# Kernel optimization log

Measured on AMD Instinct MI355X. Metric: run time of the kernel, lower is better.

Reference implementation:

```python
import jax, jax.numpy as jnp
import numpy as np

N_BLOCKS = 12   # grid rows == cols
D = 256         # per-block feature size (small -> memory-bound)
BATCH = 8192    # samples per block

# Deterministic block-sparse pattern: block (i, j) is active iff (i - j) % 3 == 0.
_mask = np.array([[(i - j) % 3 == 0 for j in range(N_BLOCKS)] for i in range(N_BLOCKS)])
_I, _J = np.nonzero(_mask)  # 48 active blocks
N_ACTIVE = _I.shape[0]


def setup_inputs() -> dict:
    key = jax.random.key(0)
    k1, k2, k3 = jax.random.split(key, 3)
    X = jax.random.normal(k1, (N_BLOCKS, BATCH, D), dtype=jnp.float32)
    # One Linear(D, D) per active block: weight [K, D_in, D_out], bias [K, D_out]
    W = jax.random.normal(k2, (N_ACTIVE, D, D), dtype=jnp.float32) / np.sqrt(D).astype(np.float32)
    b = jax.random.normal(k3, (N_ACTIVE, D), dtype=jnp.float32) * 0.01
    i_idx = jnp.asarray(_I, dtype=jnp.int32)  # output-row index of each active block
    j_idx = jnpim if False else jnp.asarray(_J, dtype=jnp.int32)  # input-col index of each active block
    return {"X": X, "W": W, "b": b, "i_idx": i_idx, "j_idx": j_idx}


def reference(X, W, b, i_idx, j_idx):
    # Gather the input block feeding each active sub-module: [K, BATCH, D]
    Xg = X[j_idx]
    # Apply each block's Linear in one batched contraction: [K, BATCH, D]
    h = jnp.einsum('kbi,kio->kbo', Xg, W) + b[:, None, :]
    # Sum block outputs into their output rows (the '+' combiner / safe_sum):
    # rows with no active block get an all-zero output, matching the zero-vector semantics.
    y = jax.ops.segment_sum(h, i_idx, num_segments=N_BLOCKS)  # [N_BLOCKS, BATCH, D]
    return y
```

## Files before the change

kernel.cpp:

```cpp
#include <hip/hip_runtime.h>

#define N_BLOCKS 12
#define D 256
#define BATCH 8192

typedef __attribute__((ext_vector_type(8))) short bf16x8;
typedef __attribute__((ext_vector_type(16))) float f32x16;

__device__ __forceinline__ unsigned short f2bf(float f) {
  unsigned int u = __float_as_uint(f);
  u += 0x7fffu + ((u >> 16) & 1u);
  return (unsigned short)(u >> 16);
}

__device__ __forceinline__ void gld16(const unsigned short* g, unsigned short* l) {
  __builtin_amdgcn_global_load_lds(
      (const __attribute__((address_space(1))) unsigned int*)g,
      (__attribute__((address_space(3))) unsigned int*)l,
      16, 0, 0);
}

__global__ void cvt_x(const float* __restrict__ X, unsigned short* __restrict__ Xb) {
  const long long t = (long long)blockIdx.x * 256 + threadIdx.x;
  const long long base = t * 8;
  const float4 v0 = *(const float4*)(X + base);
  const float4 v1 = *(const float4*)(X + base + 4);
  uint4 r;
  r.x = (unsigned)f2bf(v0.x) | ((unsigned)f2bf(v0.y) << 16);
  r.y = (unsigned)f2bf(v0.z) | ((unsigned)f2bf(v0.w) << 16);
  r.z = (unsigned)f2bf(v1.x) | ((unsigned)f2bf(v1.y) << 16);
  r.w = (unsigned)f2bf(v1.z) | ((unsigned)f2bf(v1.w) << 16);
  *(uint4*)(Xb + base) = r;
}

__global__ void cvt_w(const float* __restrict__ W, unsigned short* __restrict__ Wt) {
  __shared__ unsigned short tile[32][33];
  const int k  = blockIdx.x >> 6;
  const int t  = blockIdx.x & 63;
  const int ti = t >> 3;
  const int tj = t & 7;
  const float* Wk = W + (long long)k * D * D;
  unsigned short* Wtk = Wt + (long long)k * D * D;
  const int lx = threadIdx.x & 31, ly = threadIdx.x >> 5;
  #pragma unroll
  for (int r = 0; r < 4; ++r) {
    const int i = ti * 32 + ly + r * 8;
    const int o = tj * 32 + lx;
    tile[ly + r * 8][lx] = f2bf(Wk[i * D + o]);
  }
  __syncthreads();
  #pragma unroll
  for (int r = 0; r < 4; ++r) {
    const int o = tj * 32 + ly + r * 8;
    const int i = ti * 32 + lx;
    Wtk[o * D + i] = tile[lx][ly + r * 8];
  }
}

__launch_bounds__(256, 2)
__global__ void bs_gemm(const unsigned short* __restrict__ Xb,
                        const unsigned short* __restrict__ Wt,
                        const float* __restrict__ bias,
                        const int* __restrict__ i_idx,
                        const int* __restrict__ j_idx,
                        int nact,
                        float* __restrict__ Y) {
  __shared__ unsigned short lds[3 * 12288];

  const int bid = blockIdx.x;
  const int x   = bid & 7;
  const int loc = bid >> 3;
  const int bm  = x * 4 + (loc & 3);
  const int pp  = loc >> 2;
  const int i   = pp >> 1;
  const int bn  = pp & 1;

  int ks0 = 0, ks1 = 0, ks2 = 0, ks3 = 0, js0 = 0, js1 = 0, js2 = 0, js3 = 0, nk = 0;
  for (int k = 0; k < nact; ++k) {
    if (i_idx[k] == i) {
      const int j = j_idx[k];
      if      (nk == 0) { ks0 = k; js0 = j; }
      else if (nk == 1) { ks1 = k; js1 = j; }
      else if (nk == 2) { ks2 = k; js2 = j; }
      else              { ks3 = k; js3 = j; }
      ++nk;
    }
  }
#define JS(t) ((t) == 0 ? js0 : (t) == 1 ? js1 : (t) == 2 ? js2 : js3)
#define KS(t) ((t) == 0 ? ks0 : (t) == 1 ? ks1 : (t) == 2 ? ks2 : ks3)

  const int tid  = threadIdx.x;
  const int wave = tid >> 6;
  const int lane = tid & 63;
  const int wm   = wave >> 1;
  const int wn   = wave & 1;
  const int l31  = lane & 31;
  const int lh   = lane >> 5;

  const int g_off = (tid >> 2) * D + (((tid & 3) ^ ((tid >> 3) & 3)) * 8);

  const int sw = (l31 >> 1) & 3;
  const int cko0 = ((0 + lh) ^ sw) << 4;
  const int cko1 = ((2 + lh) ^ sw) << 4;
  const int aBase = (wm * 128 + l31) * 64;
  const int bBase = 16384 + (wn * 64 + l31) * 64;

  auto STAGE = [&](int st) {
    const int t  = st >> 3;
    const int kk = st & 7;
    unsigned short* sl = lds + (st % 3) * 12288;
    const unsigned short* As =
        Xb + ((long long)JS(t) * BATCH + bm * 256) * D + kk * 32 + g_off;
    const unsigned short* Bs =
        Wt + ((long long)KS(t) * D + bn * 128) * D + kk * 32 + g_off;
    gld16(As,           sl + tid * 8);
    gld16(As +  64 * D, sl + 2048  + tid * 8);
    gld16(As + 128 * D, sl + 4096  + tid * 8);
    gld16(As + 192 * D, sl + 6144  + tid * 8);
    gld16(Bs,           sl + 8192  + tid * 8);
    gld16(Bs +  64 * D, sl + 10240 + tid * 8);
  };

  f32x16 acc[4][2] = {};

  STAGE(0); STAGE(1);

  #pragma unroll
  for (int kt = 0; kt < 32; ++kt) {
    if (kt < 31) asm volatile("s_waitcnt vmcnt(6)" ::: "memory");
    else         asm volatile("s_waitcnt vmcnt(0)" ::: "memory");
    __builtin_amdgcn_s_barrier();
    __builtin_amdgcn_sched_barrier(0);

    const char* sb = (const char*)lds + (kt % 3) * 24576;
    bf16x8 aF[2][4], bF[2][2];
    #pragma unroll
    for (int mf = 0; mf < 4; ++mf) {
      aF[0][mf] = *(const bf16x8*)(sb + aBase + mf * 2048 + cko0);
      aF[1][mf] = *(const bf16x8*)(sb + aBase + mf * 2048 + cko1);
    }
    #pragma unroll
    for (int nf = 0; nf < 2; ++nf) {
      bF[0][nf] = *(const bf16x8*)(sb + bBase + nf * 2048 + cko0);
      bF[1][nf] = *(const bf16x8*)(sb + bBase + nf * 2048 + cko1);
    }

    if (kt < 30) STAGE(kt + 2);

    asm volatile("s_waitcnt lgkmcnt(0)" ::: "memory");
    __builtin_amdgcn_sched_barrier(0);

    __builtin_amdgcn_s_setprio(1);
    #pragma unroll
    for (int kh = 0; kh < 2; ++kh)
      #pragma unroll
      for (int mf = 0; mf < 4; ++mf)
        #pragma unroll
        for (int nf = 0; nf < 2; ++nf)
          acc[mf][nf] = __builtin_amdgcn_mfma_f32_32x32x16_bf16(
              aF[kh][mf], bF[kh][nf], acc[mf][nf], 0, 0, 0);
    __builtin_amdgcn_s_setprio(0);
  }

  float* Yb = Y + (long long)i * BATCH * D;
  const int m0 = bm * 256 + wm * 128;
  const int n0 = bn * 128 + wn * 64 + l31;
  float bsum[2];
  #pragma unroll
  for (int nf = 0; nf < 2; ++nf) {
    float s = 0.f;
    for (int t = 0; t < nk; ++t) s += bias[KS(t) * D + n0 + nf * 32];
    bsum[nf] = s;
  }
  #pragma unroll
  for (int nf = 0; nf < 2; ++nf)
    #pragma unroll
    for (int mf = 0; mf < 4; ++mf)
      #pragma unroll
      for (int rg = 0; rg < 16; ++rg) {
        const int row = (rg & 3) + 8 * (rg >> 2) + 4 * lh;
        Yb[(long long)(m0 + mf * 32 + row) * D + (n0 + nf * 32)] =
            acc[mf][nf][rg] + bsum[nf];
      }
#undef JS
#undef KS
}

extern "C" void kernel_launch(void* const* d_in, const int* in_sizes, int n_in,
                              void* d_out, int out_size, void* d_ws, size_t ws_size,
                              hipStream_t stream) {
  const float* X = (const float*)d_in[0];
  const float* W = (const float*)d_in[1];
  const float* b = (const float*)d_in[2];
  const int* i_idx = (const int*)d_in[3];
  const int* j_idx = (const int*)d_in[4];
  float* Y = (float*)d_out;
  const int nact = in_sizes[3];

  unsigned short* Xb = (unsigned short*)d_ws;
  unsigned short* Wt = (unsigned short*)((char*)d_ws + (size_t)N_BLOCKS * BATCH * D * 2);

  cvt_x<<<(N_BLOCKS * BATCH * D) / (256 * 8), 256, 0, stream>>>(X, Xb);
  cvt_w<<<nact * 64, 256, 0, stream>>>(W, Wt);
  bs_gemm<<<768, 256, 0, stream>>>(Xb, Wt, b, i_idx, j_idx, nact, Y);
}
```

Baseline: 249.4 us.

## Fuse X bf16 conversion into GEMM A-loads via register staging

Drops the separate cvt_x kernel. The GEMM now loads fp32 X tiles into registers, converts them to bf16, and writes them to LDS, using a double-buffered register-to-LDS pipeline in place of the triple-buffered direct global-to-LDS loads. This removes a full write and re-read of a bf16 copy of X plus one kernel launch. In exchange, each GEMM block reads twice the A bytes in fp32, holds more registers, and X rows are re-read by each bn tile and each of the four contributing blocks. The weight transpose kernel is also reworked to use 64x64 tiles with vector loads and stores.

New measurement: 302.7 us. 1.21x slower.

```diff
diff --git a/kernel.cpp b/kernel.cpp
--- a/kernel.cpp
+++ b/kernel.cpp
@@ -11,6 +11,10 @@
   unsigned int u = __float_as_uint(f);
   u += 0x7fffu + ((u >> 16) & 1u);
   return (unsigned short)(u >> 16);
+}
+
+__device__ __forceinline__ unsigned int pk2(float a, float b) {
+  return (unsigned)f2bf(a) | ((unsigned)f2bf(b) << 16);
 }
 
 __device__ __forceinline__ void gld16(const unsigned short* g, unsigned short* l) {
@@ -20,52 +24,45 @@
       16, 0, 0);
 }
 
-__global__ void cvt_x(const float* __restrict__ X, unsigned short* __restrict__ Xb) {
-  const long long t = (long long)blockIdx.x * 256 + threadIdx.x;
-  const long long base = t * 8;
-  const float4 v0 = *(const float4*)(X + base);
-  const float4 v1 = *(const float4*)(X + base + 4);
-  uint4 r;
-  r.x = (unsigned)f2bf(v0.x) | ((unsigned)f2bf(v0.y) << 16);
-  r.y = (unsigned)f2bf(v0.z) | ((unsigned)f2bf(v0.w) << 16);
-  r.z = (unsigned)f2bf(v1.x) | ((unsigned)f2bf(v1.y) << 16);
-  r.w = (unsigned)f2bf(v1.z) | ((unsigned)f2bf(v1.w) << 16);
-  *(uint4*)(Xb + base) = r;
-}
-
 __global__ void cvt_w(const float* __restrict__ W, unsigned short* __restrict__ Wt) {
-  __shared__ unsigned short tile[32][33];
-  const int k  = blockIdx.x >> 6;
-  const int t  = blockIdx.x & 63;
-  const int ti = t >> 3;
-  const int tj = t & 7;
+  __shared__ unsigned short T[64][72];
+  const int b  = blockIdx.x;
+  const int k  = b >> 4;
+  const int ti = (b >> 2) & 3;
+  const int tj = b & 3;
   const float* Wk = W + (long long)k * D * D;
   unsigned short* Wtk = Wt + (long long)k * D * D;
-  const int lx = threadIdx.x & 31, ly = threadIdx.x >> 5;
-  #pragma unroll
-  for (int r = 0; r < 4; ++r) {
-    const int i = ti * 32 + ly + r * 8;
-    const int o = tj * 32 + lx;
-    tile[ly + r * 8][lx] = f2bf(Wk[i * D + o]);
+  const int t = threadIdx.x;
+
+  #pragma unroll
+  for (int p = 0; p < 4; ++p) {
+    const int il = (t >> 4) + p * 16;
+    const int o4 = (t & 15) * 4;
+    const float4 v = *(const float4*)(Wk + (ti * 64 + il) * D + tj * 64 + o4);
+    T[o4 + 0][il] = f2bf(v.x);
+    T[o4 + 1][il] = f2bf(v.y);
+    T[o4 + 2][il] = f2bf(v.z);
+    T[o4 + 3][il] = f2bf(v.w);
   }
   __syncthreads();
-  #pragma unroll
-  for (int r = 0; r < 4; ++r) {
-    const int o = tj * 32 + ly + r * 8;
-    const int i = ti * 32 + lx;
-    Wtk[o * D + i] = tile[lx][ly + r * 8];
+
+  #pragma unroll
+  for (int q = 0; q < 2; ++q) {
+    const int ol = t >> 2;
+    const int i8 = (t & 3) * 8 + q * 32;
+    *(uint4*)(Wtk + (tj * 64 + ol) * D + ti * 64 + i8) = *(const uint4*)(&T[ol][i8]);
   }
 }
 
 __launch_bounds__(256, 2)
-__global__ void bs_gemm(const unsigned short* __restrict__ Xb,
+__global__ void bs_gemm(const float* __restrict__ X,
                         const unsigned short* __restrict__ Wt,
                         const float* __restrict__ bias,
                         const int* __restrict__ i_idx,
                         const int* __restrict__ j_idx,
                         int nact,
                         float* __restrict__ Y) {
-  __shared__ unsigned short lds[3 * 12288];
+  __shared__ unsigned short lds[2 * 12288];
 
   const int bid = blockIdx.x;
   const int x   = bid & 7;
@@ -97,42 +94,72 @@
   const int l31  = lane & 31;
   const int lh   = lane >> 5;
 
+  const int srow = tid >> 2;
+  const int scnk = tid & 3;
+  const int cpos = scnk ^ ((tid >> 3) & 3);
+
   const int g_off = (tid >> 2) * D + (((tid & 3) ^ ((tid >> 3) & 3)) * 8);
 
-  const int sw = (l31 >> 1) & 3;
+  const int sw   = (l31 >> 1) & 3;
   const int cko0 = ((0 + lh) ^ sw) << 4;
   const int cko1 = ((2 + lh) ^ sw) << 4;
   const int aBase = (wm * 128 + l31) * 64;
   const int bBase = 16384 + (wn * 64 + l31) * 64;
 
-  auto STAGE = [&](int st) {
+  float4 rA[8];
+
+  auto A_ISSUE = [&](int st) {
     const int t  = st >> 3;
     const int kk = st & 7;
-    unsigned short* sl = lds + (st % 3) * 12288;
-    const unsigned short* As =
-        Xb + ((long long)JS(t) * BATCH + bm * 256) * D + kk * 32 + g_off;
+    const float* base = X + ((long long)JS(t) * BATCH + bm * 256) * D
+                          + kk * 32 + scnk * 8;
+    #pragma unroll
+    for (int sb = 0; sb < 4; ++sb) {
+      const float4* p = (const float4*)(base + (long long)(srow + 64 * sb) * D);
+      rA[2 * sb]     = p[0];
+      rA[2 * sb + 1] = p[1];
+    }
+  };
+  auto A_WRITE = [&](int st) {
+    unsigned short* sl = lds + (st & 1) * 12288;
+    #pragma unroll
+    for (int sb = 0; sb < 4; ++sb) {
+      const float4 a = rA[2 * sb], b = rA[2 * sb + 1];
+      uint4 v;
+      v.x = pk2(a.x, a.y);  v.y = pk2(a.z, a.w);
+      v.z = pk2(b.x, b.y);  v.w = pk2(b.z, b.w);
+      *(uint4*)(sl + (srow + 64 * sb) * 32 + cpos * 8) = v;
+    }
+  };
+  auto STAGE_B = [&](int st) {
+    const int t  = st >> 3;
+    const int kk = st & 7;
+    unsigned short* sl = lds + (st & 1) * 12288 + 8192;
     const unsigned short* Bs =
         Wt + ((long long)KS(t) * D + bn * 128) * D + kk * 32 + g_off;
-    gld16(As,           sl + tid * 8);
-    gld16(As +  64 * D, sl + 2048  + tid * 8);
-    gld16(As + 128 * D, sl + 4096  + tid * 8);
-    gld16(As + 192 * D, sl + 6144  + tid * 8);
-    gld16(Bs,           sl + 8192  + tid * 8);
-    gld16(Bs +  64 * D, sl + 10240 + tid * 8);
+    gld16(Bs,          sl + tid * 8);
+    gld16(Bs + 64 * D, sl + 2048 + tid * 8);
   };
 
   f32x16 acc[4][2] = {};
 
-  STAGE(0); STAGE(1);
+  STAGE_B(0);
+  A_ISSUE(0);
+  __builtin_amdgcn_sched_barrier(0);
+  A_WRITE(0);
+  __builtin_amdgcn_sched_barrier(0);
+  A_ISSUE(1);
+  __builtin_amdgcn_sched_barrier(0);
+  asm volatile("s_waitcnt lgkmcnt(0)" ::: "memory");
 
   #pragma unroll
   for (int kt = 0; kt < 32; ++kt) {
-    if (kt < 31) asm volatile("s_waitcnt vmcnt(6)" ::: "memory");
-    else         asm volatile("s_waitcnt vmcnt(0)" ::: "memory");
     __builtin_amdgcn_s_barrier();
     __builtin_amdgcn_sched_barrier(0);
 
-    const char* sb = (const char*)lds + (kt % 3) * 24576;
+    if (kt < 31) STAGE_B(kt + 1);
+
+    const char* sb = (const char*)lds + (kt & 1) * 24576;
     bf16x8 aF[2][4], bF[2][2];
     #pragma unroll
     for (int mf = 0; mf < 4; ++mf) {
@@ -144,8 +171,6 @@
       bF[0][nf] = *(const bf16x8*)(sb + bBase + nf * 2048 + cko0);
       bF[1][nf] = *(const bf16x8*)(sb + bBase + nf * 2048 + cko1);
     }
-
-    if (kt < 30) STAGE(kt + 2);
 
     asm volatile("s_waitcnt lgkmcnt(0)" ::: "memory");
     __builtin_amdgcn_sched_barrier(0);
@@ -160,6 +185,15 @@
           acc[mf][nf] = __builtin_amdgcn_mfma_f32_32x32x16_bf16(
               aF[kh][mf], bF[kh][nf], acc[mf][nf], 0, 0, 0);
     __builtin_amdgcn_s_setprio(0);
+
+    if (kt < 31) A_WRITE(kt + 1);
+    __builtin_amdgcn_sched_barrier(0);
+    if (kt < 30) A_ISSUE(kt + 2);
+    __builtin_amdgcn_sched_barrier(0);
+
+    if (kt < 30)       asm volatile("s_waitcnt vmcnt(8)" ::: "memory");
+    else if (kt == 30) asm volatile("s_waitcnt vmcnt(0)" ::: "memory");
+    if (kt < 31) asm volatile("s_waitcnt lgkmcnt(0)" ::: "memory");
   }
 
   float* Yb = Y + (long long)i * BATCH * D;
@@ -197,10 +231,8 @@
   float* Y = (float*)d_out;
   const int nact = in_sizes[3];
 
-  unsigned short* Xb = (unsigned short*)d_ws;
-  unsigned short* Wt = (unsigned short*)((char*)d_ws + (size_t)N_BLOCKS * BATCH * D * 2);
-
-  cvt_x<<<(N_BLOCKS * BATCH * D) / (256 * 8), 256, 0, stream>>>(X, Xb);
-  cvt_w<<<nact * 64, 256, 0, stream>>>(W, Wt);
-  bs_gemm<<<768, 256, 0, stream>>>(Xb, Wt, b, i_idx, j_idx, nact, Y);
-}
+  unsigned short* Wt = (unsigned short*)d_ws;
+
+  cvt_w<<<768, 256, 0, stream>>>(W, Wt);
+  bs_gemm<<<768, 256, 0, stream>>>(X, Wt, b, i_idx, j_idx, nact, Y);
+}
```
